# Kernel optimization log

Measured on AMD Instinct MI355X. Metric: run time of the kernel, lower is better.

Reference implementation:

```python
import jax, jax.numpy as jnp
import numpy as np

N, E, F_IN, H, C = 50000, 800000, 128, 4, 73
HC = H * C  # 292
NEG_SLOPE_ATT = 0.2   # GATv2 attention leaky relu
NEG_SLOPE_ACT = 0.01  # F.leaky_relu default
BN_EPS = 1e-5


def setup_inputs() -> dict:
    key = jax.random.key(0)
    ks = jax.random.split(key, 20)
    rn = lambda k, shp, s=0.05: (jax.random.normal(k, shp, jnp.float32) * s)
    inp = {
        'x': jax.random.normal(ks[0], (N, F_IN), jnp.float32),
        'edge_index': jax.random.randint(ks[1], (2, E), 0, N, jnp.int64),
        # conv1 (in=F_IN)
        'Wl1': rn(ks[2], (HC, F_IN)), 'bl1': rn(ks[3], (HC,)),
        'Wr1': rn(ks[4], (HC, F_IN)), 'br1': rn(ks[5], (HC,)),
        'att1': rn(ks[6], (H, C)), 'b1': rn(ks[7], (HC,)),
        # conv2 (in=HC)
        'Wl2': rn(ks[8], (HC, HC)), 'bl2': rn(ks[9], (HC,)),
        'Wr2': rn(ks[10], (HC, HC)), 'br2': rn(ks[11], (HC,)),
        'att2': rn(ks[12], (H, C)), 'b2': rn(ks[13], (HC,)),
        # shared BatchNorm1d(HC)
        'gamma': jnp.ones((HC,), jnp.float32), 'beta': jnp.zeros((HC,), jnp.float32),
        # classifier Linear(HC, 2)
        'Wc': rn(ks[14], (2, HC)), 'bc': rn(ks[15], (2,)),
    }
    return inp


def _gatv2(x, src, dst, Wl, bl, Wr, br, att, b):
    # lin_l on source, lin_r on target (PyG GATv2Conv, share_weights=False)
    xl = (x @ Wl.T + bl).reshape(-1, H, C)  # [N,H,C]
    xr = (x @ Wr.T + br).reshape(-1, H, C)
    f = xl[src] + xr[dst]                    # [E,H,C] edge-wise gather
    s = jnp.einsum('ehc,hc->eh', jax.nn.leaky_relu(f, NEG_SLOPE_ATT), att)
    # segment softmax over incoming edges of each destination node
    m = jax.ops.segment_max(s, dst, num_segments=N)
    ex = jnp.exp(s - m[dst])
    den = jax.ops.segment_sum(ex, dst, num_segments=N)
    alpha = ex / (den[dst] + 1e-16)          # [E,H]
    out = jax.ops.segment_sum(alpha[:, :, None] * xl[src], dst, num_segments=N)
    return out.reshape(-1, HC) + b           # concat heads + bias


def _bn(x, gamma, beta):
    mu = jnp.mean(x, axis=0)
    var = jnp.mean((x - mu) ** 2, axis=0)
    return (x - mu) * jax.lax.rsqrt(var + BN_EPS) * gamma + beta


def reference(x, edge_index, Wl1, bl1, Wr1, br1, att1, b1,
              Wl2, bl2, Wr2, br2, att2, b2, gamma, beta, Wc, bc):
    src, dst = edge_index[0], edge_index[1]
    h = _gatv2(x, src, dst, Wl1, bl1, Wr1, br1, att1, b1)
    h = jax.nn.leaky_relu(_bn(h, gamma, beta), NEG_SLOPE_ACT)
    h = _gatv2(h, src, dst, Wl2, bl2, Wr2, br2, att2, b2)
    h = jax.nn.leaky_relu(_bn(h, gamma, beta), NEG_SLOPE_ACT)
    return h @ Wc.T + bc
```

## Files before the change

kernel.cpp:

```cpp
#include <hip/hip_runtime.h>

#define HCDIM 292
#define NHEAD 4
#define CDIM 73
#define SLOTS 5
#define NPERM 320
#define BN_EPS 1e-5f

using u16x8 = __attribute__((ext_vector_type(8))) unsigned short;
using s16x8 = __attribute__((ext_vector_type(8))) short;
using f32x4 = __attribute__((ext_vector_type(4))) float;
using u16x4 = __attribute__((ext_vector_type(4))) unsigned short;

__device__ inline ushort f2bf(float f) {
  unsigned int u = __float_as_uint(f);
  u += 0x7FFFu + ((u >> 16) & 1u);
  return (ushort)(u >> 16);
}
__device__ inline float bf2f(ushort v) {
  return __uint_as_float(((unsigned int)v) << 16);
}

__device__ inline int perm2feat(int p, bool& valid) {
  int h, c;
  if (p < 256) {
    h = p >> 6;
    c = ((p & 3) << 4) | ((p >> 2) & 15);
    valid = true;
  } else {
    int q = p - 256;
    h = q >> 4;
    c = 64 + (q & 15);
    valid = (q & 15) < (CDIM - 64);
  }
  return h * CDIM + c;
}

__global__ void k_zero_i32(int* __restrict__ p, int n) {
  int i = blockIdx.x * blockDim.x + threadIdx.x;
  if (i < n) p[i] = 0;
}
__global__ void k_zero_f32(float* __restrict__ p, int n) {
  int i = blockIdx.x * blockDim.x + threadIdx.x;
  if (i < n) p[i] = 0.f;
}

__global__ void k_cvt(const float* __restrict__ src, ushort* __restrict__ dst,
                      int total) {
  int i = blockIdx.x * blockDim.x + threadIdx.x;
  if (i < total) dst[i] = f2bf(src[i]);
}

__global__ void k_wperm(const float* __restrict__ W, const float* __restrict__ b,
                        ushort* __restrict__ Wp, float* __restrict__ pb,
                        int Kin, int Kpad, int kperm) {
  int p = blockIdx.x, t = threadIdx.x;
  bool pv;
  int gn = perm2feat(p, pv);
  int gk = t;
  bool kv = t < Kin;
  if (kperm) { bool v2; gk = perm2feat(t, v2); kv = v2; }
  ushort v = 0;
  if (pv && kv) v = f2bf(W[(size_t)gn * Kin + gk]);
  Wp[(size_t)p * Kpad + t] = v;
  if (t == 0) pb[p] = pv ? b[gn] : 0.f;
}

__global__ void k_vecperm(const float* __restrict__ att1, const float* __restrict__ b1,
                          const float* __restrict__ att2, const float* __restrict__ b2,
                          const float* __restrict__ gamma, const float* __restrict__ beta,
                          const float* __restrict__ Wc, float* __restrict__ o) {
  int p = threadIdx.x, w = blockIdx.x;
  bool pv;
  int gn = perm2feat(p, pv);
  const float* src;
  switch (w) {
    case 0: src = att1; break;
    case 1: src = b1; break;
    case 2: src = att2; break;
    case 3: src = b2; break;
    case 4: src = gamma; break;
    case 5: src = beta; break;
    case 6: src = Wc; break;
    default: src = Wc + HCDIM; break;
  }
  o[w * NPERM + p] = pv ? src[gn] : 0.f;
}

__global__ void k_hist(const int* __restrict__ dst, int* __restrict__ deg, int E) {
  int i = blockIdx.x * blockDim.x + threadIdx.x;
  if (i < E) atomicAdd(&deg[dst[i]], 1);
}

__global__ __launch_bounds__(256) void k_block_sum(const int* __restrict__ deg,
                                                   int* __restrict__ bsum, int n) {
  __shared__ int s[256];
  int i = blockIdx.x * 256 + threadIdx.x;
  s[threadIdx.x] = (i < n) ? deg[i] : 0;
  __syncthreads();
  for (int off = 128; off > 0; off >>= 1) {
    if (threadIdx.x < off) s[threadIdx.x] += s[threadIdx.x + off];
    __syncthreads();
  }
  if (threadIdx.x == 0) bsum[blockIdx.x] = s[0];
}

__global__ __launch_bounds__(256) void k_scan_small(const int* __restrict__ bsum,
                                                    int* __restrict__ boff, int G) {
  __shared__ int s[256];
  int t = threadIdx.x;
  int v = (t < G) ? bsum[t] : 0;
  s[t] = v;
  __syncthreads();
  for (int off = 1; off < 256; off <<= 1) {
    int tv = (t >= off) ? s[t - off] : 0;
    __syncthreads();
    s[t] += tv;
    __syncthreads();
  }
  if (t < G) boff[t] = s[t] - v;
}

__global__ __launch_bounds__(256) void k_scan_final(const int* __restrict__ deg,
                                                    const int* __restrict__ boff,
                                                    int* __restrict__ row_ptr,
                                                    int* __restrict__ cursor,
                                                    int n, int E) {
  __shared__ int s[256];
  int t = threadIdx.x;
  int i = blockIdx.x * 256 + t;
  int v = (i < n) ? deg[i] : 0;
  s[t] = v;
  __syncthreads();
  for (int off = 1; off < 256; off <<= 1) {
    int tv = (t >= off) ? s[t - off] : 0;
    __syncthreads();
    s[t] += tv;
    __syncthreads();
  }
  if (i < n) {
    int rp = boff[blockIdx.x] + s[t] - v;
    row_ptr[i] = rp;
    cursor[i] = rp;
  }
  if (i == 0) row_ptr[n] = E;
}

__global__ void k_csr_fill(const int* __restrict__ srcs, const int* __restrict__ dsts,
                           int* __restrict__ cursor, int* __restrict__ csr_src, int E) {
  int i = blockIdx.x * blockDim.x + threadIdx.x;
  if (i < E) {
    int pos = atomicAdd(&cursor[dsts[i]], 1);
    csr_src[pos] = srcs[i];
  }
}

template <int KS>
__global__ __launch_bounds__(256) void k_gemm_direct(
    const ushort* __restrict__ A, const ushort* __restrict__ Wb,
    const float* __restrict__ pb, ushort* __restrict__ o0,
    ushort* __restrict__ o1, int M, int mt) {
  int b = blockIdx.x;
  int x = b & 7, g = b >> 3;
  int ct = g & 3, mq = g >> 2;
  int m = mq * 8 + x;
  if (m >= mt) return;
  const int bm = m * 128;
  ushort* out = (ct < 2) ? o0 : o1;
  const int colbase = (ct & 1) * 160;
  const int wrow0 = ct * 160;
  const int tid = threadIdx.x;
  const int wave = tid >> 6, lane = tid & 63;
  const int quad = lane >> 4, lr = lane & 15;
  const int wm = (wave & 1) * 64, wn = (wave >> 1) * 80;

  f32x4 acc[4][5] = {};

  const ushort* Arow[4];
  const ushort* Brow[5];
#pragma unroll
  for (int i = 0; i < 4; ++i) {
    int ar = bm + wm + i * 16 + lr;
    if (ar >= M) ar = M - 1;
    Arow[i] = A + (size_t)ar * KS;
  }
#pragma unroll
  for (int i = 0; i < 5; ++i)
    Brow[i] = Wb + (size_t)(wrow0 + wn + i * 16 + lr) * KS;

#pragma unroll
  for (int k0 = 0; k0 < KS; k0 += 32) {
    s16x8 af[4], bf[5];
#pragma unroll
    for (int i = 0; i < 4; ++i)
      af[i] = *(const s16x8*)(Arow[i] + k0 + quad * 8);
#pragma unroll
    for (int i = 0; i < 5; ++i)
      bf[i] = *(const s16x8*)(Brow[i] + k0 + quad * 8);
#pragma unroll
    for (int mi = 0; mi < 4; ++mi)
#pragma unroll
      for (int ni = 0; ni < 5; ++ni)
        acc[mi][ni] = __builtin_amdgcn_mfma_f32_16x16x32_bf16(af[mi], bf[ni],
                                                              acc[mi][ni], 0, 0, 0);
  }

  float pbv[5];
#pragma unroll
  for (int ni = 0; ni < 5; ++ni) pbv[ni] = pb[wrow0 + wn + ni * 16 + lr];

#pragma unroll
  for (int mi = 0; mi < 4; ++mi) {
#pragma unroll
    for (int r = 0; r < 4; ++r) {
      int gm = bm + wm + mi * 16 + quad * 4 + r;
      if (gm >= M) continue;
#pragma unroll
      for (int ni = 0; ni < 5; ++ni) {
        int gn = colbase + wn + ni * 16 + lr;
        out[(size_t)gm * NPERM + gn] = f2bf(acc[mi][ni][r] + pbv[ni]);
      }
    }
  }
}

__global__ __launch_bounds__(256) void k_pre(const ushort* __restrict__ xl,
                                             const float* __restrict__ attp,
                                             float* __restrict__ pl, int n) {
  int wave = threadIdx.x >> 6, lane = threadIdx.x & 63;
  int d = blockIdx.x * 4 + wave;
  if (d >= n) return;
  int hgrp = lane >> 4, li = lane & 15;
  u16x4 a4 = *(const u16x4*)(xl + (size_t)d * NPERM + lane * 4);
  ushort a1 = xl[(size_t)d * NPERM + 256 + lane];
  float Ta = 0.f;
#pragma unroll
  for (int k = 0; k < 4; ++k) Ta = fmaf(bf2f(a4[k]), attp[lane * 4 + k], Ta);
  Ta = fmaf(bf2f(a1), attp[256 + lane], Ta);
#pragma unroll
  for (int off = 1; off < 16; off <<= 1) Ta += __shfl_xor(Ta, off, 64);
  if (li == 0) pl[d * 4 + hgrp] = 0.6f * Ta;
}

__global__ __launch_bounds__(256) void k_agg(const ushort* __restrict__ xl,
                                             const ushort* __restrict__ xr,
                                             const float* __restrict__ pl,
                                             const int* __restrict__ csr_src,
                                             const int* __restrict__ row_ptr,
                                             const float* __restrict__ attp,
                                             const float* __restrict__ bp,
                                             ushort* __restrict__ out, int n) {
  int wave = threadIdx.x >> 6, lane = threadIdx.x & 63;
  int d = blockIdx.x * 4 + wave;
  if (d >= n) return;
  int hgrp = lane >> 4;
  int start = __builtin_amdgcn_readfirstlane(row_ptr[d]);
  int end = __builtin_amdgcn_readfirstlane(row_ptr[d + 1]);

  float bpv[SLOTS];
#pragma unroll
  for (int k = 0; k < 4; ++k) bpv[k] = bp[lane * 4 + k];
  bpv[4] = bp[256 + lane];

  if (start >= end) {
    u16x4 o4;
#pragma unroll
    for (int k = 0; k < 4; ++k) o4[k] = f2bf(bpv[k]);
    *(u16x4*)(out + (size_t)d * NPERM + lane * 4) = o4;
    out[(size_t)d * NPERM + 256 + lane] = f2bf(bpv[4]);
    return;
  }

  float xrv[SLOTS], attv[SLOTS], acc[SLOTS] = {};
  {
    u16x4 r4 = *(const u16x4*)(xr + (size_t)d * NPERM + lane * 4);
#pragma unroll
    for (int k = 0; k < 4; ++k) {
      xrv[k] = bf2f(r4[k]);
      attv[k] = 0.4f * attp[lane * 4 + k];
    }
    xrv[4] = bf2f(xr[(size_t)d * NPERM + 256 + lane]);
    attv[4] = 0.4f * attp[256 + lane];
  }
  float Tb = 0.f;
#pragma unroll
  for (int k = 0; k < SLOTS; ++k) Tb = fmaf(xrv[k], attv[k], Tb);
  Tb += __shfl_xor(Tb, 1, 64);
  Tb += __shfl_xor(Tb, 2, 64);
  Tb += __shfl_xor(Tb, 4, 64);
  Tb += __shfl_xor(Tb, 8, 64);
  float prv = 1.5f * Tb;
  float den = 0.f;
  int dg = end - start;

  int sA = __builtin_amdgcn_readfirstlane(csr_src[start]);
  int eB0 = (dg > 1) ? start + 1 : start;
  int sB = __builtin_amdgcn_readfirstlane(csr_src[eB0]);
  u16x4 a4 = *(const u16x4*)(xl + (size_t)sA * NPERM + lane * 4);
  ushort a1 = xl[(size_t)sA * NPERM + 256 + lane];
  float plA = pl[sA * 4 + hgrp];
  u16x4 b4 = *(const u16x4*)(xl + (size_t)sB * NPERM + lane * 4);
  ushort b1 = xl[(size_t)sB * NPERM + 256 + lane];
  float plB = pl[sB * 4 + hgrp];

  for (int e = start; e + 1 < end; e += 2) {
    int p0 = (e + 2 < end) ? e + 2 : end - 1;
    int p1 = (e + 3 < end) ? e + 3 : end - 1;
    int t0 = __builtin_amdgcn_readfirstlane(csr_src[p0]);
    int t1 = __builtin_amdgcn_readfirstlane(csr_src[p1]);
    u16x4 n4a = *(const u16x4*)(xl + (size_t)t0 * NPERM + lane * 4);
    ushort n1a = xl[(size_t)t0 * NPERM + 256 + lane];
    float plN0 = pl[t0 * 4 + hgrp];
    u16x4 n4b = *(const u16x4*)(xl + (size_t)t1 * NPERM + lane * 4);
    ushort n1b = xl[(size_t)t1 * NPERM + 256 + lane];
    float plN1 = pl[t1 * 4 + hgrp];

    float xa[SLOTS] = {bf2f(a4[0]), bf2f(a4[1]), bf2f(a4[2]), bf2f(a4[3]), bf2f(a1)};
    float xb[SLOTS] = {bf2f(b4[0]), bf2f(b4[1]), bf2f(b4[2]), bf2f(b4[3]), bf2f(b1)};
    float Ta = 0.f, Tc = 0.f;
#pragma unroll
    for (int k = 0; k < SLOTS; ++k) {
      Ta = fmaf(fabsf(xa[k] + xrv[k]), attv[k], Ta);
      Tc = fmaf(fabsf(xb[k] + xrv[k]), attv[k], Tc);
    }
    Ta += __shfl_xor(Ta, 1, 64);  Tc += __shfl_xor(Tc, 1, 64);
    Ta += __shfl_xor(Ta, 2, 64);  Tc += __shfl_xor(Tc, 2, 64);
    Ta += __shfl_xor(Ta, 4, 64);  Tc += __shfl_xor(Tc, 4, 64);
    Ta += __shfl_xor(Ta, 8, 64);  Tc += __shfl_xor(Tc, 8, 64);
    float sa_ = fminf(Ta + plA + prv, 60.f);
    float sb_ = fminf(Tc + plB + prv, 60.f);
    float wa = __expf(sa_);
    float wb = __expf(sb_);
    den += wa + wb;
#pragma unroll
    for (int k = 0; k < SLOTS; ++k) {
      acc[k] = fmaf(wa, xa[k], acc[k]);
      acc[k] = fmaf(wb, xb[k], acc[k]);
    }
    a4 = n4a; a1 = n1a; plA = plN0;
    b4 = n4b; b1 = n1b; plB = plN1;
  }

  if (dg & 1) {
    float xa[SLOTS] = {bf2f(a4[0]), bf2f(a4[1]), bf2f(a4[2]), bf2f(a4[3]), bf2f(a1)};
    float Ta = 0.f;
#pragma unroll
    for (int k = 0; k < SLOTS; ++k)
      Ta = fmaf(fabsf(xa[k] + xrv[k]), attv[k], Ta);
    Ta += __shfl_xor(Ta, 1, 64);
    Ta += __shfl_xor(Ta, 2, 64);
    Ta += __shfl_xor(Ta, 4, 64);
    Ta += __shfl_xor(Ta, 8, 64);
    float wa = __expf(fminf(Ta + plA + prv, 60.f));
    den += wa;
#pragma unroll
    for (int k = 0; k < SLOTS; ++k) acc[k] = fmaf(wa, xa[k], acc[k]);
  }

  float inv = 1.f / (den + 1e-16f);
  u16x4 o4;
#pragma unroll
  for (int k = 0; k < 4; ++k) o4[k] = f2bf(fmaf(acc[k], inv, bpv[k]));
  *(u16x4*)(out + (size_t)d * NPERM + lane * 4) = o4;
  out[(size_t)d * NPERM + 256 + lane] = f2bf(fmaf(acc[4], inv, bpv[4]));
}

__global__ __launch_bounds__(320) void k_bn_reduce(const ushort* __restrict__ h,
                                                   float* __restrict__ colsum,
                                                   float* __restrict__ colsq,
                                                   int n, int rows_per_block) {
  int c = threadIdx.x;
  int r0 = blockIdx.x * rows_per_block;
  int r1 = min(r0 + rows_per_block, n);
  float s = 0.f, s2 = 0.f;
  for (int r = r0; r < r1; ++r) {
    float v = bf2f(h[(size_t)r * NPERM + c]);
    s += v;
    s2 += v * v;
  }
  atomicAdd(&colsum[c], s);
  atomicAdd(&colsq[c], s2);
}

__global__ void k_bn_coef(float* __restrict__ colsum, float* __restrict__ colsq,
                          const float* __restrict__ gp, const float* __restrict__ bp,
                          float invN) {
  int c = threadIdx.x + blockIdx.x * blockDim.x;
  if (c >= NPERM) return;
  float mu = colsum[c] * invN;
  float var = colsq[c] * invN - mu * mu;
  float scale = rsqrtf(var + BN_EPS) * gp[c];
  colsum[c] = scale;
  colsq[c] = bp[c] - mu * scale;
}

__global__ void k_bn_apply_bf(const ushort* __restrict__ h,
                              const float* __restrict__ scale,
                              const float* __restrict__ shift,
                              ushort* __restrict__ outb, int total8) {
  int i = blockIdx.x * blockDim.x + threadIdx.x;
  if (i >= total8) return;
  int cg = i - (i / 40) * 40;
  u16x8 v = *(const u16x8*)(h + (size_t)i * 8);
  u16x8 o;
#pragma unroll
  for (int k = 0; k < 8; ++k) {
    int c = cg * 8 + k;
    float f = fmaf(bf2f(v[k]), scale[c], shift[c]);
    f = (f > 0.f) ? f : 0.01f * f;
    o[k] = f2bf(f);
  }
  *(u16x8*)(outb + (size_t)i * 8) = o;
}

__global__ __launch_bounds__(256) void k_bn_classifier(
    const ushort* __restrict__ h, const float* __restrict__ scale,
    const float* __restrict__ shift, const float* __restrict__ wc0,
    const float* __restrict__ wc1, const float* __restrict__ bc,
    float* __restrict__ out, int n) {
  int wave = threadIdx.x >> 6, lane = threadIdx.x & 63;
  int r = blockIdx.x * 4 + wave;
  if (r >= n) return;
  float a0 = 0.f, a1 = 0.f;
#pragma unroll
  for (int k = 0; k < SLOTS; ++k) {
    int slot = lane + 64 * k;
    float v = fmaf(bf2f(h[(size_t)r * NPERM + slot]), scale[slot], shift[slot]);
    v = (v > 0.f) ? v : 0.01f * v;
    a0 = fmaf(v, wc0[slot], a0);
    a1 = fmaf(v, wc1[slot], a1);
  }
#pragma unroll
  for (int off = 32; off > 0; off >>= 1) {
    a0 += __shfl_xor(a0, off, 64);
    a1 += __shfl_xor(a1, off, 64);
  }
  if (lane == 0) {
    out[(size_t)2 * r] = a0 + bc[0];
    out[(size_t)2 * r + 1] = a1 + bc[1];
  }
}

extern "C" void kernel_launch(void* const* d_in, const int* in_sizes, int n_in,
                              void* d_out, int out_size, void* d_ws, size_t ws_size,
                              hipStream_t stream) {
  const float* x      = (const float*)d_in[0];
  const int*   eidx   = (const int*)d_in[1];
  const float* Wl1    = (const float*)d_in[2];
  const float* bl1    = (const float*)d_in[3];
  const float* Wr1    = (const float*)d_in[4];
  const float* br1    = (const float*)d_in[5];
  const float* att1   = (const float*)d_in[6];
  const float* b1     = (const float*)d_in[7];
  const float* Wl2    = (const float*)d_in[8];
  const float* bl2    = (const float*)d_in[9];
  const float* Wr2    = (const float*)d_in[10];
  const float* br2    = (const float*)d_in[11];
  const float* att2   = (const float*)d_in[12];
  const float* b2     = (const float*)d_in[13];
  const float* gamma  = (const float*)d_in[14];
  const float* beta   = (const float*)d_in[15];
  const float* Wc     = (const float*)d_in[16];
  const float* bc     = (const float*)d_in[17];
  float* out = (float*)d_out;

  const int FIN = 128;
  const int N = in_sizes[0] / FIN;
  const int E = in_sizes[1] / 2;

  const int* src = eidx;
  const int* dst = eidx + E;

  ushort* h      = (ushort*)d_ws;
  ushort* xl     = h + (size_t)N * NPERM;
  ushort* xr     = xl + (size_t)N * NPERM;
  ushort* abuf   = xr + (size_t)N * NPERM;
  ushort* wb     = abuf + (size_t)N * NPERM;
  float* pb      = (float*)(wb + (size_t)2 * NPERM * NPERM);
  float* vecp    = pb + 2 * NPERM;
  float* pl      = vecp + 8 * NPERM;
  float* colsum  = pl + (size_t)N * NHEAD;
  float* colsq   = colsum + NPERM;
  int* deg       = (int*)(colsq + NPERM);
  int* row_ptr   = deg + N;
  int* cursor    = row_ptr + N + 1;
  int* bsum      = cursor + N;
  int* boff      = bsum + 256;
  int* csr_src   = boff + 256;

  const int G = (N + 255) / 256;
  const int EB = (E + 255) / 256;
  const int AGGB = (N + 3) / 4;
  const int mt = (N + 127) / 128;
  const int GEMMB = 8 * 4 * ((mt + 7) / 8);

  const float* att1p = vecp;
  const float* b1p   = vecp + NPERM;
  const float* att2p = vecp + 2 * NPERM;
  const float* b2p   = vecp + 3 * NPERM;
  const float* gp    = vecp + 4 * NPERM;
  const float* btp   = vecp + 5 * NPERM;
  const float* wc0   = vecp + 6 * NPERM;
  const float* wc1   = vecp + 7 * NPERM;

  k_zero_i32<<<G, 256, 0, stream>>>(deg, N);
  k_hist<<<EB, 256, 0, stream>>>(dst, deg, E);
  k_block_sum<<<G, 256, 0, stream>>>(deg, bsum, N);
  k_scan_small<<<1, 256, 0, stream>>>(bsum, boff, G);
  k_scan_final<<<G, 256, 0, stream>>>(deg, boff, row_ptr, cursor, N, E);
  k_csr_fill<<<EB, 256, 0, stream>>>(src, dst, cursor, csr_src, E);

  k_vecperm<<<8, NPERM, 0, stream>>>(att1, b1, att2, b2, gamma, beta, Wc, vecp);

  k_cvt<<<(N * FIN + 255) / 256, 256, 0, stream>>>(x, abuf, N * FIN);
  k_wperm<<<NPERM, FIN, 0, stream>>>(Wl1, bl1, wb, pb, FIN, FIN, 0);
  k_wperm<<<NPERM, FIN, 0, stream>>>(Wr1, br1, wb + (size_t)NPERM * FIN, pb + NPERM,
                                     FIN, FIN, 0);
  k_gemm_direct<FIN><<<GEMMB, 256, 0, stream>>>(abuf, wb, pb, xl, xr, N, mt);
  k_pre<<<AGGB, 256, 0, stream>>>(xl, att1p, pl, N);
  k_agg<<<AGGB, 256, 0, stream>>>(xl, xr, pl, csr_src, row_ptr, att1p, b1p, h, N);

  const int RPB = (N + 255) / 256;
  k_zero_f32<<<1, 2 * NPERM, 0, stream>>>(colsum, 2 * NPERM);
  k_bn_reduce<<<256, NPERM, 0, stream>>>(h, colsum, colsq, N, RPB);
  k_bn_coef<<<2, 160, 0, stream>>>(colsum, colsq, gp, btp, 1.f / (float)N);
  k_bn_apply_bf<<<(N * 40 + 255) / 256, 256, 0, stream>>>(h, colsum, colsq, abuf,
                                                          N * 40);

  k_wperm<<<NPERM, NPERM, 0, stream>>>(Wl2, bl2, wb, pb, HCDIM, NPERM, 1);
  k_wperm<<<NPERM, NPERM, 0, stream>>>(Wr2, br2, wb + (size_t)NPERM * NPERM,
                                       pb + NPERM, HCDIM, NPERM, 1);
  k_gemm_direct<NPERM><<<GEMMB, 256, 0, stream>>>(abuf, wb, pb, xl, xr, N, mt);
  k_pre<<<AGGB, 256, 0, stream>>>(xl, att2p, pl, N);
  k_agg<<<AGGB, 256, 0, stream>>>(xl, xr, pl, csr_src, row_ptr, att2p, b2p, h, N);

  k_zero_f32<<<1, 2 * NPERM, 0, stream>>>(colsum, 2 * NPERM);
  k_bn_reduce<<<256, NPERM, 0, stream>>>(h, colsum, colsq, N, RPB);
  k_bn_coef<<<2, 160, 0, stream>>>(colsum, colsq, gp, btp, 1.f / (float)N);

  k_bn_classifier<<<AGGB, 256, 0, stream>>>(h, colsum, colsq, wc0, wc1, bc, out, N);
}
```

Baseline: 641.4 us.

## Fuse input bf16 conversion into GEMM, double-buffer fragments, vectorize output stores

Removes the separate fp32-to-bf16 conversion kernel for the first layer input by converting inside the GEMM fragment loads. Adds double-buffered fragment loading so global loads for the next k-step overlap MFMA work. Swaps MFMA operand order so each lane holds four consecutive output columns, enabling packed 4-element bf16 stores and vector bias loads. The first GEMM now reads fp32 input directly, doubling its A-read bytes, and extra register pressure is a risk.

```diff
diff --git a/kernel.cpp b/kernel.cpp
--- a/kernel.cpp
+++ b/kernel.cpp
@@ -43,12 +43,6 @@
 __global__ void k_zero_f32(float* __restrict__ p, int n) {
   int i = blockIdx.x * blockDim.x + threadIdx.x;
   if (i < n) p[i] = 0.f;
-}
-
-__global__ void k_cvt(const float* __restrict__ src, ushort* __restrict__ dst,
-                      int total) {
-  int i = blockIdx.x * blockDim.x + threadIdx.x;
-  if (i < total) dst[i] = f2bf(src[i]);
 }
 
 __global__ void k_wperm(const float* __restrict__ W, const float* __restrict__ b,
@@ -155,9 +149,44 @@
   }
 }
 
-template <int KS>
+template <bool CVT>
+__device__ inline void load_frags(const char* const (&Ar)[4],
+                                  const ushort* const (&Br)[5], int koff, int quad,
+                                  s16x8 (&af)[4], s16x8 (&bf)[5]) {
+#pragma unroll
+  for (int i = 0; i < 4; ++i) {
+    if (CVT) {
+      const float* p = (const float*)Ar[i] + koff + quad * 8;
+      float4 f0 = *(const float4*)p;
+      float4 f1 = *(const float4*)(p + 4);
+      s16x8 v;
+      v[0] = (short)f2bf(f0.x); v[1] = (short)f2bf(f0.y);
+      v[2] = (short)f2bf(f0.z); v[3] = (short)f2bf(f0.w);
+      v[4] = (short)f2bf(f1.x); v[5] = (short)f2bf(f1.y);
+      v[6] = (short)f2bf(f1.z); v[7] = (short)f2bf(f1.w);
+      af[i] = v;
+    } else {
+      af[i] = *(const s16x8*)((const ushort*)Ar[i] + koff + quad * 8);
+    }
+  }
+#pragma unroll
+  for (int i = 0; i < 5; ++i)
+    bf[i] = *(const s16x8*)(Br[i] + koff + quad * 8);
+}
+
+__device__ inline void mfma_block(const s16x8 (&af)[4], const s16x8 (&bf)[5],
+                                  f32x4 (&acc)[4][5]) {
+#pragma unroll
+  for (int mi = 0; mi < 4; ++mi)
+#pragma unroll
+    for (int ni = 0; ni < 5; ++ni)
+      acc[mi][ni] = __builtin_amdgcn_mfma_f32_16x16x32_bf16(bf[ni], af[mi],
+                                                            acc[mi][ni], 0, 0, 0);
+}
+
+template <int KS, bool CVT>
 __global__ __launch_bounds__(256) void k_gemm_direct(
-    const ushort* __restrict__ A, const ushort* __restrict__ Wb,
+    const void* __restrict__ Av, const ushort* __restrict__ Wb,
     const float* __restrict__ pb, ushort* __restrict__ o0,
     ushort* __restrict__ o1, int M, int mt) {
   int b = blockIdx.x;
@@ -176,50 +205,45 @@
 
   f32x4 acc[4][5] = {};
 
-  const ushort* Arow[4];
-  const ushort* Brow[5];
+  const char* Ar[4];
+  const ushort* Br[5];
+  const int esz = CVT ? 4 : 2;
 #pragma unroll
   for (int i = 0; i < 4; ++i) {
     int ar = bm + wm + i * 16 + lr;
     if (ar >= M) ar = M - 1;
-    Arow[i] = A + (size_t)ar * KS;
+    Ar[i] = (const char*)Av + (size_t)ar * KS * esz;
   }
 #pragma unroll
   for (int i = 0; i < 5; ++i)
-    Brow[i] = Wb + (size_t)(wrow0 + wn + i * 16 + lr) * KS;
-
-#pragma unroll
-  for (int k0 = 0; k0 < KS; k0 += 32) {
-    s16x8 af[4], bf[5];
-#pragma unroll
-    for (int i = 0; i < 4; ++i)
-      af[i] = *(const s16x8*)(Arow[i] + k0 + quad * 8);
-#pragma unroll
-    for (int i = 0; i < 5; ++i)
-      bf[i] = *(const s16x8*)(Brow[i] + k0 + quad * 8);
-#pragma unroll
-    for (int mi = 0; mi < 4; ++mi)
-#pragma unroll
-      for (int ni = 0; ni < 5; ++ni)
-        acc[mi][ni] = __builtin_amdgcn_mfma_f32_16x16x32_bf16(af[mi], bf[ni],
-                                                              acc[mi][ni], 0, 0, 0);
-  }
-
-  float pbv[5];
-#pragma unroll
-  for (int ni = 0; ni < 5; ++ni) pbv[ni] = pb[wrow0 + wn + ni * 16 + lr];
+    Br[i] = Wb + (size_t)(wrow0 + wn + i * 16 + lr) * KS;
+
+  s16x8 afA[4], bfA[5], afB[4], bfB[5];
+  load_frags<CVT>(Ar, Br, 0, quad, afA, bfA);
+#pragma unroll
+  for (int k0 = 0; k0 < KS; k0 += 64) {
+    if (k0 + 32 < KS) load_frags<CVT>(Ar, Br, k0 + 32, quad, afB, bfB);
+    mfma_block(afA, bfA, acc);
+    if (k0 + 32 < KS) {
+      if (k0 + 64 < KS) load_frags<CVT>(Ar, Br, k0 + 64, quad, afA, bfA);
+      mfma_block(afB, bfB, acc);
+    }
+  }
 
 #pragma unroll
   for (int mi = 0; mi < 4; ++mi) {
-#pragma unroll
-    for (int r = 0; r < 4; ++r) {
-      int gm = bm + wm + mi * 16 + quad * 4 + r;
-      if (gm >= M) continue;
-#pragma unroll
-      for (int ni = 0; ni < 5; ++ni) {
-        int gn = colbase + wn + ni * 16 + lr;
-        out[(size_t)gm * NPERM + gn] = f2bf(acc[mi][ni][r] + pbv[ni]);
-      }
+    int gm = bm + wm + mi * 16 + lr;
+    if (gm >= M) continue;
+    ushort* orow = out + (size_t)gm * NPERM + colbase + wn + quad * 4;
+#pragma unroll
+    for (int ni = 0; ni < 5; ++ni) {
+      float4 pbv = *(const float4*)(pb + wrow0 + wn + ni * 16 + quad * 4);
+      u16x4 o;
+      o[0] = f2bf(acc[mi][ni][0] + pbv.x);
+      o[1] = f2bf(acc[mi][ni][1] + pbv.y);
+      o[2] = f2bf(acc[mi][ni][2] + pbv.z);
+      o[3] = f2bf(acc[mi][ni][3] + pbv.w);
+      *(u16x4*)(orow + ni * 16) = o;
     }
   }
 }
@@ -512,11 +536,11 @@
 
   k_vecperm<<<8, NPERM, 0, stream>>>(att1, b1, att2, b2, gamma, beta, Wc, vecp);
 
-  k_cvt<<<(N * FIN + 255) / 256, 256, 0, stream>>>(x, abuf, N * FIN);
   k_wperm<<<NPERM, FIN, 0, stream>>>(Wl1, bl1, wb, pb, FIN, FIN, 0);
   k_wperm<<<NPERM, FIN, 0, stream>>>(Wr1, br1, wb + (size_t)NPERM * FIN, pb + NPERM,
                                      FIN, FIN, 0);
-  k_gemm_direct<FIN><<<GEMMB, 256, 0, stream>>>(abuf, wb, pb, xl, xr, N, mt);
+  k_gemm_direct<FIN, true><<<GEMMB, 256, 0, stream>>>((const void*)x, wb, pb,
+                                                      xl, xr, N, mt);
   k_pre<<<AGGB, 256, 0, stream>>>(xl, att1p, pl, N);
   k_agg<<<AGGB, 256, 0, stream>>>(xl, xr, pl, csr_src, row_ptr, att1p, b1p, h, N);
 
@@ -530,7 +554,8 @@
   k_wperm<<<NPERM, NPERM, 0, stream>>>(Wl2, bl2, wb, pb, HCDIM, NPERM, 1);
   k_wperm<<<NPERM, NPERM, 0, stream>>>(Wr2, br2, wb + (size_t)NPERM * NPERM,
                                        pb + NPERM, HCDIM, NPERM, 1);
-  k_gemm_direct<NPERM><<<GEMMB, 256, 0, stream>>>(abuf, wb, pb, xl, xr, N, mt);
+  k_gemm_direct<NPERM, false><<<GEMMB, 256, 0, stream>>>((const void*)abuf, wb, pb,
+                                                         xl, xr, N, mt);
   k_pre<<<AGGB, 256, 0, stream>>>(xl, att2p, pl, N);
   k_agg<<<AGGB, 256, 0, stream>>>(xl, xr, pl, csr_src, row_ptr, att2p, b2p, h, N);
 
```

Measured after the change: 657.4 us. +2.5%, slower.
